# Kernel tuning notes

Measured on AMD Instinct MI355X. Metric: run time of the kernel, lower is better.

The kernel has to match this reference:

```python
import jax, jax.numpy as jnp
import numpy as np

NEG = -1e9

def setup_inputs() -> dict:
    key = jax.random.key(0)
    kx, kq, kk, kv, kbq, kbk, kbv = jax.random.split(key, 7)
    B, S, E, D = 4, 2048, 1024, 64
    x = jax.random.normal(kx, (B, S, E), dtype=jnp.float32)
    # causal mask, broadcast over batch (mask == 0 positions get -1e9)
    mask = jnp.broadcast_to(jnp.tril(jnp.ones((S, S), dtype=jnp.int32)), (B, S, S))
    scale = 1.0 / np.sqrt(E)
    Wq = jax.random.normal(kq, (E, D), dtype=jnp.float32) * scale
    Wk = jax.random.normal(kk, (E, D), dtype=jnp.float32) * scale
    Wv = jax.random.normal(kv, (E, D), dtype=jnp.float32) * scale
    bq = jnp.zeros((D,), dtype=jnp.float32)
    bk = jnp.zeros((D,), dtype=jnp.float32)
    bv = jnp.zeros((D,), dtype=jnp.float32)
    return {"x": x, "mask": mask, "Wq": Wq, "bq": bq, "Wk": Wk, "bk": bk, "Wv": Wv, "bv": bv}

def reference(x, mask, Wq, bq, Wk, bk, Wv, bv):
    # Faithful to original: forward passes (K(x), Q(x), V(x)) into sdpa,
    # so the K-projection plays the 'query' role and Q-projection the 'key' role.
    q = jnp.einsum('bse,ed->bsd', x, Wk) + bk  # K(x) used as queries
    k = jnp.einsum('bse,ed->bsd', x, Wq) + bq  # Q(x) used as keys
    v = jnp.einsum('bse,ed->bsd', x, Wv) + bv
    d = q.shape[-1]
    scores = jnp.einsum('bsd,btd->bst', q, k) / jnp.sqrt(jnp.asarray(d, q.dtype))
    scores = jnp.where(mask == 0, jnp.asarray(NEG, scores.dtype), scores)
    weights = jax.nn.softmax(scores, axis=-1)
    return jnp.einsum('bst,btd->bsd', weights, v)
```

## Files before the change

### kernel.cpp

```cpp
#include <hip/hip_runtime.h>

typedef short bf16x8 __attribute__((ext_vector_type(8)));
typedef float f32x4  __attribute__((ext_vector_type(4)));
typedef int   i32x4  __attribute__((ext_vector_type(4)));

#define NEG_BIG (-1e9f)

__device__ __forceinline__ float bf2f(unsigned short h){
  union { unsigned u; float f; } v; v.u = ((unsigned)h) << 16; return v.f;
}
__device__ __forceinline__ unsigned short f2bf(float f){
  union { float f; unsigned u; } v; v.f = f;
  unsigned u = v.u;
  return (unsigned short)((u + 0x7FFFu + ((u >> 16) & 1u)) >> 16);
}

__global__ __launch_bounds__(256) void prep_kernel(
    const float* __restrict__ Wq, const float* __restrict__ bq,
    const float* __restrict__ Wk, const float* __restrict__ bk,
    const float* __restrict__ Wv, const float* __restrict__ bv,
    unsigned short* __restrict__ Wimg, float* __restrict__ bias)
{
  int idx = blockIdx.x * 256 + threadIdx.x;
  if (idx < 192 * 1024) {
    int kb2 = idx / 24576, rem = idx % 24576;
    int r = rem >> 7, kk = rem & 127;
    int k = kb2 * 128 + kk;
    float v;
    if (r < 64)       v = Wk[k * 64 + r];
    else if (r < 128) v = Wq[k * 64 + (r - 64)];
    else              v = Wv[k * 64 + (r - 128)];
    Wimg[kb2 * 24576 + r * 128 + kk] = f2bf(v);
  }
  if (idx < 192) {
    float b;
    if (idx < 64)       b = bk[idx];
    else if (idx < 128) b = bq[idx - 64];
    else                b = bv[idx - 128];
    bias[idx] = b;
  }
}

__global__ __launch_bounds__(256, 2) void proj_kernel(
    const float* __restrict__ x,
    const unsigned short* __restrict__ Wimg,
    const float* __restrict__ bias,
    unsigned short* __restrict__ Qh,
    unsigned short* __restrict__ Kh, unsigned short* __restrict__ Vth)
{
  __shared__ __align__(16) unsigned short Axb[32 * 128];
  __shared__ __align__(16) unsigned short Wc[96 * 128];

  const int tid  = threadIdx.x;
  const int lane = tid & 63;
  const int w    = tid >> 6;
  const int rh   = w & 1;
  const int cg   = w >> 1;
  const int quad = lane >> 4;
  const int li   = lane & 15;
  const int rowbase = (blockIdx.x >> 1) * 32;
  const int ch      = blockIdx.x & 1;

  const int xr0 = tid >> 4,          xc0 = tid & 15;
  const int xr1 = (tid + 256) >> 4,  xc1 = tid & 15;
  const float* agp0 = x + (size_t)(rowbase + xr0) * 1024 + xc0 * 8;
  const float* agp1 = x + (size_t)(rowbase + xr1) * 1024 + xc1 * 8;
  const int aslot0 = xr0 * 128 + (xc0 ^ (xr0 & 15)) * 8;
  const int aslot1 = xr1 * 128 + (xc1 ^ (xr1 & 15)) * 8;

  int wslot[6];
  const unsigned short* wgp[6];
  #pragma unroll
  for (int j = 0; j < 6; j++) {
    int cid = tid + j * 256;
    int wr = cid >> 4, c = cid & 15;
    wslot[j] = wr * 128 + (c ^ (wr & 15)) * 8;
    wgp[j] = Wimg + (size_t)(ch * 96 + wr) * 128 + c * 8;
  }

  f32x4 acc[3];
  #pragma unroll
  for (int c = 0; c < 3; c++) acc[c] = (f32x4){0.f, 0.f, 0.f, 0.f};

  const int alr = rh * 16 + li;

  f32x4 rA[4];
  rA[0] = *(const f32x4*)(agp0);
  rA[1] = *(const f32x4*)(agp0 + 4);
  rA[2] = *(const f32x4*)(agp1);
  rA[3] = *(const f32x4*)(agp1 + 4);
  i32x4 rW[6];
  #pragma unroll
  for (int j = 0; j < 6; j++) rW[j] = *(const i32x4*)(wgp[j]);

  for (int ks = 0; ks < 8; ks++) {
    bf16x8 xa, xb;
    #pragma unroll
    for (int j = 0; j < 4; j++) {
      xa[j]     = f2bf(rA[0][j]);
      xa[4 + j] = f2bf(rA[1][j]);
      xb[j]     = f2bf(rA[2][j]);
      xb[4 + j] = f2bf(rA[3][j]);
    }
    __syncthreads();
    *(bf16x8*)&Axb[aslot0] = xa;
    *(bf16x8*)&Axb[aslot1] = xb;
    #pragma unroll
    for (int j = 0; j < 6; j++) *(i32x4*)&Wc[wslot[j]] = rW[j];
    if (ks < 7) {
      rA[0] = *(const f32x4*)(agp0 + (ks + 1) * 128);
      rA[1] = *(const f32x4*)(agp0 + (ks + 1) * 128 + 4);
      rA[2] = *(const f32x4*)(agp1 + (ks + 1) * 128);
      rA[3] = *(const f32x4*)(agp1 + (ks + 1) * 128 + 4);
      #pragma unroll
      for (int j = 0; j < 6; j++)
        rW[j] = *(const i32x4*)(wgp[j] + (size_t)(ks + 1) * 24576);
    }
    __syncthreads();

    #pragma unroll
    for (int sub = 0; sub < 4; sub++) {
      bf16x8 af = *(const bf16x8*)&Axb[alr * 128 + ((sub * 4 + quad) ^ (alr & 15)) * 8];
      #pragma unroll
      for (int ct = 0; ct < 3; ct++) {
        const int lw = cg * 48 + ct * 16 + li;
        bf16x8 bf = *(const bf16x8*)&Wc[lw * 128 + ((sub * 4 + quad) ^ (lw & 15)) * 8];
        acc[ct] = __builtin_amdgcn_mfma_f32_16x16x32_bf16(af, bf, acc[ct], 0, 0, 0);
      }
    }
  }

  if (ch == 0) {
    #pragma unroll
    for (int ct = 0; ct < 3; ct++)
      #pragma unroll
      for (int r = 0; r < 4; r++) {
        int row = rowbase + rh * 16 + quad * 4 + r;
        int col = cg * 48 + ct * 16 + li;
        unsigned short h = f2bf(acc[ct][r] + bias[col]);
        if (col < 64) Qh[(size_t)row * 64 + col] = h;
        else          Kh[(size_t)row * 64 + (col - 64)] = h;
      }
  } else {
    __syncthreads();
    unsigned short* Vlds = Wc;
    #pragma unroll
    for (int ct = 0; ct < 3; ct++)
      #pragma unroll
      for (int r = 0; r < 4; r++) {
        int srow = rh * 16 + quad * 4 + r;
        int col = 96 + cg * 48 + ct * 16 + li;
        unsigned short h = f2bf(acc[ct][r] + bias[col]);
        if (col < 128) Kh[(size_t)(rowbase + srow) * 64 + (col - 64)] = h;
        else           Vlds[(col - 128) * 40 + srow] = h;
      }
    __syncthreads();
    const int d  = tid >> 2;
    const int sc = tid & 3;
    bf16x8 vv = *(const bf16x8*)&Vlds[d * 40 + sc * 8];
    const int grow = rowbase;
    const int bb = grow >> 11, s0 = (grow & 2047) + sc * 8;
    *(bf16x8*)&Vth[(size_t)bb * 131072 + (size_t)d * 2048 + s0] = vv;
  }
}

__global__ __launch_bounds__(256, 3) void attn_part_kernel(
    const unsigned short* __restrict__ Qh,
    const unsigned short* __restrict__ Kh,
    const unsigned short* __restrict__ Vth,
    float* __restrict__ pacc, float* __restrict__ pl,
    float* __restrict__ out)
{
  __shared__ __align__(16) unsigned short Kst[2][64 * 64];
  __shared__ __align__(16) unsigned short Vst[2][64 * 64];
  __shared__ __align__(16) unsigned short Ps[4][16 * 72];

  const int tid  = threadIdx.x;
  const int lane = tid & 63;
  const int w    = tid >> 6;
  const int quad = lane >> 4;
  const int li   = lane & 15;

  const int b = blockIdx.x / 144;
  int r = blockIdx.x % 144;
  int qg = 31, part = 0;
  #pragma unroll 1
  for (int g = 31; g >= 0; g--) {
    int Pg = (g + 4) >> 2;
    if (r < Pg) { qg = g; part = r; break; }
    r -= Pg;
  }
  const int nkt = qg + 1;
  const int P   = (qg + 4) >> 2;
  const int base = nkt / P, rem = nkt % P;
  const int kt0 = part * base + (part < rem ? part : rem);
  const int kt1 = kt0 + base + (part < rem ? 1 : 0);
  const int qbase = qg * 64 + w * 16;

  size_t qoff = ((size_t)(b * 2048 + qbase) + li) * 64 + quad * 8;
  bf16x8 qh0 = *(const bf16x8*)(Qh + qoff);
  bf16x8 qh1 = *(const bf16x8*)(Qh + qoff + 32);

  f32x4 acc[4];
  #pragma unroll
  for (int c = 0; c < 4; c++) acc[c] = (f32x4){0.f, 0.f, 0.f, 0.f};
  f32x4 lacc = (f32x4){0.f, 0.f, 0.f, 0.f};

  bf16x8 ones;
  #pragma unroll
  for (int j = 0; j < 8; j++) ones[j] = (short)0x3F80;

  const int srow = tid >> 2, sc = tid & 3;
  const unsigned short* kgp = Kh + (size_t)(b * 2048 + srow) * 64 + sc * 8;
  const unsigned short* vgp = Vth + (size_t)b * 131072 + (size_t)srow * 2048 + sc * 8;
  const int ks0 = srow * 64 + ((sc)     ^ (srow & 7)) * 8;
  const int ks1 = srow * 64 + ((sc + 4) ^ (srow & 7)) * 8;

  i32x4 rk0 = *(const i32x4*)(kgp + (size_t)kt0 * 4096);
  i32x4 rk1 = *(const i32x4*)(kgp + (size_t)kt0 * 4096 + 32);
  i32x4 rv0 = *(const i32x4*)(vgp + kt0 * 64);
  i32x4 rv1 = *(const i32x4*)(vgp + kt0 * 64 + 32);

  *(i32x4*)&Kst[0][ks0] = rk0;
  *(i32x4*)&Kst[0][ks1] = rk1;
  *(i32x4*)&Vst[0][ks0] = rv0;
  *(i32x4*)&Vst[0][ks1] = rv1;
  __syncthreads();

  int cur = 0;
  for (int kt = kt0; kt < kt1; kt++) {
    const bool more = (kt + 1 < kt1);
    if (more) {
      rk0 = *(const i32x4*)(kgp + (size_t)(kt + 1) * 4096);
      rk1 = *(const i32x4*)(kgp + (size_t)(kt + 1) * 4096 + 32);
      rv0 = *(const i32x4*)(vgp + (kt + 1) * 64);
      rv1 = *(const i32x4*)(vgp + (kt + 1) * 64 + 32);
    }

    f32x4 s[4];
    #pragma unroll
    for (int c = 0; c < 4; c++) s[c] = (f32x4){0.f, 0.f, 0.f, 0.f};
    __builtin_amdgcn_s_setprio(1);
    #pragma unroll
    for (int ct = 0; ct < 4; ct++) {
      const int n = ct * 16 + li;
      bf16x8 kf0 = *(const bf16x8*)&Kst[cur][n * 64 + ((quad)     ^ (n & 7)) * 8];
      bf16x8 kf1 = *(const bf16x8*)&Kst[cur][n * 64 + ((quad + 4) ^ (n & 7)) * 8];
      s[ct] = __builtin_amdgcn_mfma_f32_16x16x32_bf16(qh0, kf0, s[ct], 0, 0, 0);
      s[ct] = __builtin_amdgcn_mfma_f32_16x16x32_bf16(qh1, kf1, s[ct], 0, 0, 0);
    }
    __builtin_amdgcn_s_setprio(0);

    const bool diag = (kt == qg);
    const int kb = kt * 64;
    #pragma unroll
    for (int ct = 0; ct < 4; ct++)
      #pragma unroll
      for (int rr = 0; rr < 4; rr++) {
        float t = fmaf(s[ct][rr], 0.18033688011112042f, -23.083120654223414f);
        if (diag && (kb + ct * 16 + li > qbase + quad * 4 + rr)) t = -1e30f;
        Ps[w][(quad * 4 + rr) * 72 + ct * 16 + li] = f2bf(exp2f(t));
      }

    bf16x8 ap0 = *(const bf16x8*)&Ps[w][li * 72 + quad * 8];
    bf16x8 ap1 = *(const bf16x8*)&Ps[w][li * 72 + 32 + quad * 8];

    __builtin_amdgcn_s_setprio(1);
    lacc = __builtin_amdgcn_mfma_f32_16x16x32_bf16(ap0, ones, lacc, 0, 0, 0);
    lacc = __builtin_amdgcn_mfma_f32_16x16x32_bf16(ap1, ones, lacc, 0, 0, 0);
    #pragma unroll
    for (int ct = 0; ct < 4; ct++) {
      const int n = ct * 16 + li;
      bf16x8 vf0 = *(const bf16x8*)&Vst[cur][n * 64 + ((quad)     ^ (n & 7)) * 8];
      bf16x8 vf1 = *(const bf16x8*)&Vst[cur][n * 64 + ((quad + 4) ^ (n & 7)) * 8];
      acc[ct] = __builtin_amdgcn_mfma_f32_16x16x32_bf16(ap0, vf0, acc[ct], 0, 0, 0);
      acc[ct] = __builtin_amdgcn_mfma_f32_16x16x32_bf16(ap1, vf1, acc[ct], 0, 0, 0);
    }
    __builtin_amdgcn_s_setprio(0);

    if (more) {
      *(i32x4*)&Kst[cur ^ 1][ks0] = rk0;
      *(i32x4*)&Kst[cur ^ 1][ks1] = rk1;
      *(i32x4*)&Vst[cur ^ 1][ks0] = rv0;
      *(i32x4*)&Vst[cur ^ 1][ks1] = rv1;
      __syncthreads();
      cur ^= 1;
    }
  }

  if (P == 1) {
    float inv[4];
    #pragma unroll
    for (int rr = 0; rr < 4; rr++) inv[rr] = 1.0f / lacc[rr];
    #pragma unroll
    for (int ct = 0; ct < 4; ct++)
      #pragma unroll
      for (int rr = 0; rr < 4; rr++)
        out[(size_t)(b * 2048 + qg * 64 + w * 16 + quad * 4 + rr) * 64 + ct * 16 + li]
          = acc[ct][rr] * inv[rr];
    return;
  }

  const int slot = (b * 32 + qg) * 8 + part;
  float* pa = pacc + (size_t)slot * 4096;
  #pragma unroll
  for (int ct = 0; ct < 4; ct++)
    #pragma unroll
    for (int rr = 0; rr < 4; rr++)
      pa[(w * 16 + quad * 4 + rr) * 64 + ct * 16 + li] = acc[ct][rr];
  if (li == 0) {
    #pragma unroll
    for (int rr = 0; rr < 4; rr++)
      pl[slot * 64 + w * 16 + quad * 4 + rr] = lacc[rr];
  }
}

__global__ __launch_bounds__(256) void attn_merge_kernel(
    const float* __restrict__ pacc, const float* __restrict__ pl,
    float* __restrict__ out)
{
  const int tid = threadIdx.x;
  const int b   = blockIdx.x / 28;
  const int qg  = (blockIdx.x % 28) + 4;
  const int rr  = tid >> 2;
  const int c0  = (tid & 3) * 16;
  const int P   = (qg + 4) >> 2;
  const int slot0 = (b * 32 + qg) * 8;

  f32x4 a0 = (f32x4){0.f,0.f,0.f,0.f}, a1 = a0, a2 = a0, a3 = a0;
  float L = 0.f;
  for (int p = 0; p < P; p++) {
    const float* pa = pacc + (size_t)(slot0 + p) * 4096 + rr * 64 + c0;
    a0 += *(const f32x4*)(pa);
    a1 += *(const f32x4*)(pa + 4);
    a2 += *(const f32x4*)(pa + 8);
    a3 += *(const f32x4*)(pa + 12);
    L += pl[(slot0 + p) * 64 + rr];
  }
  float inv = 1.f / L;
  float* o = out + ((size_t)(b * 2048 + qg * 64 + rr)) * 64 + c0;
  *(f32x4*)(o)      = a0 * inv;
  *(f32x4*)(o + 4)  = a1 * inv;
  *(f32x4*)(o + 8)  = a2 * inv;
  *(f32x4*)(o + 12) = a3 * inv;
}

extern "C" void kernel_launch(void* const* d_in, const int* in_sizes, int n_in,
                              void* d_out, int out_size, void* d_ws, size_t ws_size,
                              hipStream_t stream)
{
  (void)in_sizes; (void)n_in; (void)out_size; (void)ws_size;
  const float* x  = (const float*)d_in[0];
  const float* Wq = (const float*)d_in[2];
  const float* bq = (const float*)d_in[3];
  const float* Wk = (const float*)d_in[4];
  const float* bk = (const float*)d_in[5];
  const float* Wv = (const float*)d_in[6];
  const float* bv = (const float*)d_in[7];
  float* out = (float*)d_out;

  char* ws = (char*)d_ws;
  const size_t MB = 1u << 20;
  unsigned short* Qh   = (unsigned short*)(ws);
  unsigned short* Kh   = (unsigned short*)(ws + 2 * MB);
  unsigned short* Vth  = (unsigned short*)(ws + 4 * MB);
  unsigned short* Wimg = (unsigned short*)(ws + 6 * MB);
  float*          bias = (float*)(ws + 6 * MB + 786432);
  float*          pacc = (float*)(ws + 8 * MB);
  float*          pl   = (float*)(ws + 25 * MB);

  prep_kernel<<<dim3(768), dim3(256), 0, stream>>>(Wq, bq, Wk, bk, Wv, bv, Wimg, bias);
  proj_kernel<<<dim3(512), dim3(256), 0, stream>>>(x, Wimg, bias, Qh, Kh, Vth);
  attn_part_kernel<<<dim3(576), dim3(256), 0, stream>>>(Qh, Kh, Vth, pacc, pl, out);
  attn_merge_kernel<<<dim3(112), dim3(256), 0, stream>>>(pacc, pl, out);
}
```

Before: 150.6 us.

## Split causal attention into finer KV partitions and tile weight prep through LDS

Raises the number of key-tile partitions per query group from about one per four tiles to about one per three, giving 748 attention blocks instead of 576. The partial-sum slot stride and merge ranges are resized to match. The weight prep kernel is rewritten as a 48-block tiled transpose through shared memory with coalesced vector loads and stores, replacing scattered per-element reads. The finer split is meant to improve load balance and CU occupancy, at the cost of more partial writes and more merge traffic.

```diff
diff --git a/kernel.cpp b/kernel.cpp
--- a/kernel.cpp
+++ b/kernel.cpp
@@ -21,23 +21,47 @@
     const float* __restrict__ Wv, const float* __restrict__ bv,
     unsigned short* __restrict__ Wimg, float* __restrict__ bias)
 {
-  int idx = blockIdx.x * 256 + threadIdx.x;
-  if (idx < 192 * 1024) {
-    int kb2 = idx / 24576, rem = idx % 24576;
-    int r = rem >> 7, kk = rem & 127;
-    int k = kb2 * 128 + kk;
-    float v;
-    if (r < 64)       v = Wk[k * 64 + r];
-    else if (r < 128) v = Wq[k * 64 + (r - 64)];
-    else              v = Wv[k * 64 + (r - 128)];
-    Wimg[kb2 * 24576 + r * 128 + kk] = f2bf(v);
-  }
-  if (idx < 192) {
+  __shared__ float Wt[64][65];
+
+  const int tid = threadIdx.x;
+  const int kb2 = blockIdx.x / 6;
+  const int rem = blockIdx.x % 6;
+  const int mat = rem >> 1;
+  const int kh  = rem & 1;
+  const int kbase = kb2 * 128 + kh * 64;
+
+  const float* W = (mat == 0) ? Wk : (mat == 1) ? Wq : Wv;
+
+  #pragma unroll
+  for (int i = 0; i < 4; i++) {
+    int krow = (tid >> 4) + i * 16;
+    int d4   = (tid & 15) * 4;
+    f32x4 v = *(const f32x4*)&W[(size_t)(kbase + krow) * 64 + d4];
+    Wt[krow][d4 + 0] = v[0];
+    Wt[krow][d4 + 1] = v[1];
+    Wt[krow][d4 + 2] = v[2];
+    Wt[krow][d4 + 3] = v[3];
+  }
+  __syncthreads();
+
+  const int d = tid >> 2;
+  const int c = tid & 3;
+  const int r = mat * 64 + d;
+  #pragma unroll
+  for (int h = 0; h < 2; h++) {
+    int cc = c + h * 4;
+    bf16x8 o;
+    #pragma unroll
+    for (int i = 0; i < 8; i++) o[i] = f2bf(Wt[cc * 8 + i][d]);
+    *(bf16x8*)&Wimg[(size_t)kb2 * 24576 + r * 128 + kh * 64 + cc * 8] = o;
+  }
+
+  if (blockIdx.x == 0 && tid < 192) {
     float b;
-    if (idx < 64)       b = bk[idx];
-    else if (idx < 128) b = bq[idx - 64];
-    else                b = bv[idx - 128];
-    bias[idx] = b;
+    if (tid < 64)       b = bk[tid];
+    else if (tid < 128) b = bq[tid - 64];
+    else                b = bv[tid - 128];
+    bias[tid] = b;
   }
 }
 
@@ -181,17 +205,17 @@
   const int quad = lane >> 4;
   const int li   = lane & 15;
 
-  const int b = blockIdx.x / 144;
-  int r = blockIdx.x % 144;
+  const int b = blockIdx.x / 187;
+  int r = blockIdx.x % 187;
   int qg = 31, part = 0;
   #pragma unroll 1
   for (int g = 31; g >= 0; g--) {
-    int Pg = (g + 4) >> 2;
+    int Pg = (g + 3) / 3;
     if (r < Pg) { qg = g; part = r; break; }
     r -= Pg;
   }
   const int nkt = qg + 1;
-  const int P   = (qg + 4) >> 2;
+  const int P   = (qg + 3) / 3;
   const int base = nkt / P, rem = nkt % P;
   const int kt0 = part * base + (part < rem ? part : rem);
   const int kt1 = kt0 + base + (part < rem ? 1 : 0);
@@ -301,7 +325,7 @@
     return;
   }
 
-  const int slot = (b * 32 + qg) * 8 + part;
+  const int slot = (b * 32 + qg) * 16 + part;
   float* pa = pacc + (size_t)slot * 4096;
   #pragma unroll
   for (int ct = 0; ct < 4; ct++)
@@ -320,12 +344,12 @@
     float* __restrict__ out)
 {
   const int tid = threadIdx.x;
-  const int b   = blockIdx.x / 28;
-  const int qg  = (blockIdx.x % 28) + 4;
+  const int b   = blockIdx.x / 29;
+  const int qg  = (blockIdx.x % 29) + 3;
   const int rr  = tid >> 2;
   const int c0  = (tid & 3) * 16;
-  const int P   = (qg + 4) >> 2;
-  const int slot0 = (b * 32 + qg) * 8;
+  const int P   = (qg + 3) / 3;
+  const int slot0 = (b * 32 + qg) * 16;
 
   f32x4 a0 = (f32x4){0.f,0.f,0.f,0.f}, a1 = a0, a2 = a0, a3 = a0;
   float L = 0.f;
@@ -367,10 +391,10 @@
   unsigned short* Wimg = (unsigned short*)(ws + 6 * MB);
   float*          bias = (float*)(ws + 6 * MB + 786432);
   float*          pacc = (float*)(ws + 8 * MB);
-  float*          pl   = (float*)(ws + 25 * MB);
-
-  prep_kernel<<<dim3(768), dim3(256), 0, stream>>>(Wq, bq, Wk, bk, Wv, bv, Wimg, bias);
+  float*          pl   = (float*)(ws + 40 * MB);
+
+  prep_kernel<<<dim3(48), dim3(256), 0, stream>>>(Wq, bq, Wk, bk, Wv, bv, Wimg, bias);
   proj_kernel<<<dim3(512), dim3(256), 0, stream>>>(x, Wimg, bias, Qh, Kh, Vth);
-  attn_part_kernel<<<dim3(576), dim3(256), 0, stream>>>(Qh, Kh, Vth, pacc, pl, out);
-  attn_merge_kernel<<<dim3(112), dim3(256), 0, stream>>>(pacc, pl, out);
-}
+  attn_part_kernel<<<dim3(748), dim3(256), 0, stream>>>(Qh, Kh, Vth, pacc, pl, out);
+  attn_merge_kernel<<<dim3(116), dim3(256), 0, stream>>>(pacc, pl, out);
+}
```

Measured after the change: 149.9 us (median of 2 runs). No clear change (-0.4%).
